# Kernel tuning notes

Measured on AMD Instinct MI355X. Metric: run time of the kernel, lower is better.

Reference implementation:

```python
import jax, jax.numpy as jnp
from jax import lax
import numpy as np

B, L, IN_DIM, HID, BINS = 1, 384, 41, 64, 63
ATTN_DIM, NUM_ANCHORS = 32, 32
NUM_CONV, ATTN_EVERY = 6, 2
SIGMA, EPS = 12.0, 1e-5
DILATIONS = [1, 2, 4, 8, 16]


def select_anchors(length, k):
    # deterministic 'stride' mode of select_anchors
    k = max(1, min(k, length))
    stride = max(1, length // k)
    idx = np.arange(0, length, stride)[:k]
    if idx.size < k:
        idx = np.concatenate([idx, np.full(k - idx.size, length - 1)])
    return jnp.asarray(idx, dtype=jnp.int32)


def conv2d(x, w, b, dilation=1):
    # x: (b, Cin, H, W), w: (Cout, Cin, kh, kw) -- 'same' padding like torch padding=dilation*(k//2)
    pad = dilation * (w.shape[-1] // 2)
    y = lax.conv_general_dilated(x, w, (1, 1), [(pad, pad), (pad, pad)],
                                 rhs_dilation=(dilation, dilation),
                                 dimension_numbers=('NCHW', 'OIHW', 'NCHW'))
    return y + b[None, :, None, None]


def instance_norm(x):
    # torch InstanceNorm2d(affine=False), eps=1e-5, per (b, c) over spatial dims
    mu = x.mean(axis=(2, 3), keepdims=True)
    var = x.var(axis=(2, 3), keepdims=True)
    return (x - mu) * lax.rsqrt(var + EPS)


def anchor_attention(pair, td, tq, anchors, wq, wl, wr, wvl, wvr, wo, wg, bg,
                     tg_w1, tg_b1, tg_w2, tg_b2):
    # pair: (b, L, L, d); td: (b, L, L); tq: (b,)
    q = pair @ wq                                    # (b, L, L, a)
    p_left = pair[:, :, anchors, :]                  # (b, L, K, d)
    p_right = pair[:, anchors, :, :]                 # (b, K, L, d)
    left = p_left @ wl                               # (b, L, K, a)
    right = p_right @ wr                             # (b, K, L, a)
    scores = jnp.einsum('bija,bika->bijk', q, left)
    scores = scores + jnp.einsum('bija,bkja->bijk', q, right)
    scores = scores / jnp.sqrt(jnp.float32(ATTN_DIM))
    # template bias, 'consistency' mode
    t_left = td[:, :, anchors]                       # (b, L, K)
    t_right = jnp.swapaxes(td[:, anchors, :], 1, 2)  # (b, L, K)
    t_sum = t_left[:, :, None, :] + t_right[:, None, :, :]  # (b, L, L, K)
    bias = -jnp.abs(t_sum - td[..., None]) / SIGMA
    # TemplateGate
    coverage = (td > 0).astype(jnp.float32).mean(axis=(1, 2))        # (b,)
    length_norm = jnp.full_like(coverage, td.shape[-1] / 512.0)
    feats = jnp.stack([coverage, tq, length_norm], axis=-1)          # (b, 3)
    g = jax.nn.sigmoid(jax.nn.relu(feats @ tg_w1 + tg_b1) @ tg_w2 + tg_b2)  # (b, 1)
    scores = scores + g[:, :, None, None] * bias
    attn = jax.nn.softmax(scores, axis=-1)
    v_left = p_left @ wvl                            # (b, L, K, a)
    v_right = p_right @ wvr                          # (b, K, L, a)
    update = jnp.einsum('bijk,bika->bija', attn, v_left)
    update = update + jnp.einsum('bijk,bkja->bija', attn, v_right)
    update = update @ wo                             # (b, L, L, d)
    gate = jax.nn.sigmoid(pair @ wg + bg)
    return pair + gate * update


def setup_inputs() -> dict:
    key = jax.random.key(0)
    ks = iter(jax.random.split(key, 40))

    def rn(shape, scale=0.05):
        return jax.random.normal(next(ks), shape, dtype=jnp.float32) * scale

    return dict(
        features=jax.random.normal(next(ks), (B, L, L, IN_DIM), dtype=jnp.float32),
        template_dist=jax.random.uniform(next(ks), (B, L, L), dtype=jnp.float32) * 20.0,
        template_quality=jax.random.uniform(next(ks), (B,), dtype=jnp.float32),
        in_w=rn((HID, IN_DIM, 1, 1)), in_b=rn((HID,)),
        conv1_w=rn((NUM_CONV, HID, HID, 3, 3)), conv1_b=rn((NUM_CONV, HID)),
        conv2_w=rn((NUM_CONV, HID, HID, 3, 3)), conv2_b=rn((NUM_CONV, HID)),
        wq=rn((HID, ATTN_DIM)), wl=rn((HID, ATTN_DIM)), wr=rn((HID, ATTN_DIM)),
        wvl=rn((HID, ATTN_DIM)), wvr=rn((HID, ATTN_DIM)), wo=rn((ATTN_DIM, HID)),
        wg=rn((HID, HID)), bg=rn((HID,)),
        tg_w1=rn((3, 16)), tg_b1=rn((16,)), tg_w2=rn((16, 1)), tg_b2=rn((1,)),
        dist_w=rn((BINS, HID, 3, 3)), dist_b=rn((BINS,)),
        cf_w1=rn((32, BINS, 3, 3)), cf_b1=rn((32,)),
        cf_w2=rn((32, 32, 3, 3)), cf_b2=rn((32,)),
        cf_w3=rn((1, 32, 1, 1)), cf_b3=rn((1,)),
    )


def reference(features, template_dist, template_quality, in_w, in_b,
              conv1_w, conv1_b, conv2_w, conv2_b,
              wq, wl, wr, wvl, wvr, wo, wg, bg, tg_w1, tg_b1, tg_w2, tg_b2,
              dist_w, dist_b, cf_w1, cf_b1, cf_w2, cf_b2, cf_w3, cf_b3):
    anchors = select_anchors(L, NUM_ANCHORS)
    x = conv2d(jnp.transpose(features, (0, 3, 1, 2)), in_w, in_b)  # (b, hid, L, L)
    num_attn = max(1, NUM_CONV // max(1, ATTN_EVERY))
    attn_added = 0
    for i in range(NUM_CONV):
        d = DILATIONS[i % len(DILATIONS)]
        res = x
        out = jax.nn.elu(instance_norm(conv2d(x, conv1_w[i], conv1_b[i], d)))
        out = instance_norm(conv2d(out, conv2_w[i], conv2_b[i], 1))
        x = jax.nn.elu(out + res)
        if (i + 1) % ATTN_EVERY == 0 and attn_added < num_attn:
            pair = jnp.transpose(x, (0, 2, 3, 1))
            pair = anchor_attention(pair, template_dist, template_quality, anchors,
                                    wq, wl, wr, wvl, wvr, wo, wg, bg,
                                    tg_w1, tg_b1, tg_w2, tg_b2)
            x = jnp.transpose(pair, (0, 3, 1, 2))
            attn_added += 1
    logits = conv2d(x, dist_w, dist_b)                       # (b, bins, L, L)
    logits = 0.5 * (logits + jnp.swapaxes(logits, 2, 3))     # symmetrize_pairs
    c = jax.nn.relu(conv2d(logits, cf_w1, cf_b1))
    c = jax.nn.relu(conv2d(c, cf_w2, cf_b2))
    confidence = jax.nn.sigmoid(conv2d(c, cf_w3, cf_b3))[:, 0]   # (b, L, L)
    distance_logits = jnp.transpose(logits, (0, 2, 3, 1))        # (b, L, L, bins)
    return distance_logits, confidence
```

## Files before the change

kernel.cpp:

```cpp
#include <hip/hip_runtime.h>
#include <math.h>

#define LDIM 384
#define NPIX (LDIM*LDIM)
#define NBINS 63

typedef __attribute__((ext_vector_type(8))) __bf16 bf16x8;
typedef __attribute__((ext_vector_type(4))) float floatx4;

__device__ __forceinline__ float sigf(float x){ return 1.f/(1.f+expf(-x)); }

__global__ __launch_bounds__(256) void prep_kernel(
    const float* __restrict__ c1w, const float* __restrict__ c2w,
    const float* __restrict__ dw, const float* __restrict__ cf1w,
    const float* __restrict__ cf2w, const float* __restrict__ wg,
    const float* __restrict__ wo, const float* __restrict__ wq,
    __bf16* __restrict__ Wf){
  int idx = blockIdx.x*256 + threadIdx.x;
  if (idx >= 515072) return;
  if (idx >= 506880){
    int rel, NT, NDIM; const float* src;
    if (idx < 510976){ rel = idx - 506880; src = wg; NT=4; NDIM=64; }
    else if (idx < 513024){ rel = idx - 510976; src = wo; NT=4; NDIM=64; }
    else { rel = idx - 513024; src = wq; NT=2; NDIM=32; }
    int j = rel & 7, lane = (rel>>3) & 63;
    int r2 = rel >> 9;
    int nt = r2 % NT, kc = r2 / NT;
    int k = kc*32 + (lane>>4)*8 + j;
    int n = nt*16 + (lane&15);
    Wf[idx] = (__bf16)src[(size_t)k*NDIM + n];
    return;
  }
  const float* src; int ICreal, OCreal, ICP, NT, rel;
  if (idx < 442368){
    int layer = idx / 36864; rel = idx - layer*36864;
    int i = layer >> 1;
    src = (layer & 1) ? (c2w + (size_t)i*36864) : (c1w + (size_t)i*36864);
    ICreal=64; OCreal=64; ICP=64; NT=4;
  } else if (idx < 479232){
    rel = idx - 442368; src = dw;   ICreal=64; OCreal=63; ICP=64; NT=4;
  } else if (idx < 497664){
    rel = idx - 479232; src = cf1w; ICreal=63; OCreal=32; ICP=64; NT=2;
  } else {
    rel = idx - 497664; src = cf2w; ICreal=32; OCreal=32; ICP=32; NT=2;
  }
  int j = rel & 7, lane = (rel>>3) & 63;
  int r2 = rel >> 9;
  int nt = r2 % NT; int r3 = r2 / NT;
  int KC = ICP/32;
  int kc = r3 % KC; int tap = r3 / KC;
  int k = kc*32 + (lane>>4)*8 + j;
  int n = nt*16 + (lane&15);
  float v = 0.f;
  if (k < ICreal && n < OCreal) v = src[((size_t)n*ICreal + k)*9 + tap];
  Wf[idx] = (__bf16)v;
}

template<int ICP, int NT, int D, int WAVES, bool NORM>
__global__ __launch_bounds__(WAVES*64) void mfma_conv(
    const __bf16* __restrict__ Ain, const __bf16* __restrict__ Wf,
    const float* __restrict__ bias, int OC_real,
    float* __restrict__ outF, __bf16* __restrict__ outP,
    int relu, const float* __restrict__ nstats, float* __restrict__ ostats){
  constexpr int KC = ICP/32;
  constexpr int W = WAVES*16;
  constexpr int T = WAVES*64;
  constexpr int SW = W + 2*D;
  constexpr int REC_B = ICP*4;
  constexpr int P_B = REC_B + 8;
  constexpr int PPX = ICP/8;
  constexpr int TOT1 = SW*PPX;
  constexpr int NC1 = (TOT1 + T - 1)/T;
  constexpr int OCS = NT*16;
  const int t = threadIdx.x;
  const int wave = t>>6, lane = t&63;
  const int q = lane>>4, col16 = lane&15;
  const int y = blockIdx.y;
  const int x0 = blockIdx.x*W;
  extern __shared__ __align__(16) char smem[];
  char* stage = smem;
  float* muS = (float*)(smem + (size_t)SW*P_B);

  if (NORM){
    if (t < 64){
      float s=0.f, sq=0.f;
      #pragma unroll
      for (int rp=0;rp<8;rp++){ s += nstats[rp*128 + t]; sq += nstats[rp*128 + 64 + t]; }
      float m = s*(1.f/NPIX);
      muS[t] = m;
      muS[64+t] = rsqrtf(sq*(1.f/NPIX) - m*m + 1e-5f);
    }
    __syncthreads();
  }

  floatx4 acc[NT];
  #pragma unroll
  for (int b=0;b<NT;b++){ floatx4 z = {0.f,0.f,0.f,0.f}; acc[b]=z; }

  #pragma unroll
  for (int ky=0; ky<3; ky++){
    const int yr = y + (ky-1)*D;
    uint4 vh[NC1], vl[NC1];
    #pragma unroll
    for (int k=0;k<NC1;k++){
      uint4 z = {0u,0u,0u,0u}; vh[k]=z; vl[k]=z;
      int pp = t + k*T;
      if (pp < TOT1){
        int px = pp/PPX; int sub = pp - px*PPX;
        int gx = x0 - D + px;
        if ((unsigned)yr < LDIM && (unsigned)gx < LDIM){
          const char* p = (const char*)Ain + ((size_t)yr*LDIM + gx)*REC_B + sub*16;
          vh[k] = *(const uint4*)p;
          vl[k] = *(const uint4*)(p + ICP*2);
        }
      }
    }
    if (NORM){
      #pragma unroll
      for (int k=0;k<NC1;k++){
        int pp = t + k*T;
        if (pp < TOT1){
          int px = pp/PPX; int sub = pp - px*PPX;
          int gx = x0 - D + px;
          if ((unsigned)yr < LDIM && (unsigned)gx < LDIM){
            int c0 = sub*8;
            floatx4 mua = *(floatx4*)(muS + c0), mub = *(floatx4*)(muS + c0 + 4);
            floatx4 rsa = *(floatx4*)(muS + 64 + c0), rsb = *(floatx4*)(muS + 64 + c0 + 4);
            __bf16* hp = (__bf16*)&vh[k]; __bf16* lp = (__bf16*)&vl[k];
            #pragma unroll
            for (int j=0;j<8;j++){
              float mu = (j<4) ? mua[j] : mub[j-4];
              float rs = (j<4) ? rsa[j] : rsb[j-4];
              float v = ((float)hp[j] + (float)lp[j] - mu)*rs;
              v = v>0.f ? v : expm1f(v);
              __bf16 h = (__bf16)v; hp[j]=h; lp[j]=(__bf16)(v-(float)h);
            }
          }
        }
      }
    }
    if (ky > 0) __syncthreads();
    #pragma unroll
    for (int k=0;k<NC1;k++){
      int pp = t + k*T;
      if (pp < TOT1){
        int px = pp/PPX; int sub = pp - px*PPX;
        char* sp = stage + (size_t)px*P_B + sub*16;
        *(uint4*)sp = vh[k];
        *(uint4*)(sp + ICP*2) = vl[k];
      }
    }
    __syncthreads();
    #pragma unroll
    for (int kx=0; kx<3; kx++){
      #pragma unroll
      for (int kc=0; kc<KC; kc++){
        int cl = wave*16 + col16 + kx*D;
        const char* ap = stage + (size_t)cl*P_B + (kc*4+q)*16;
        bf16x8 ah = *(const bf16x8*)ap;
        bf16x8 al = *(const bf16x8*)(ap + ICP*2);
        const __bf16* wkc = Wf + (size_t)((ky*3+kx)*KC + kc)*NT*512 + lane*8;
        #pragma unroll
        for (int nt=0; nt<NT; nt++){
          bf16x8 bfrag = *(const bf16x8*)(wkc + (size_t)nt*512);
          acc[nt] = __builtin_amdgcn_mfma_f32_16x16x32_bf16(ah, bfrag, acc[nt], 0,0,0);
          acc[nt] = __builtin_amdgcn_mfma_f32_16x16x32_bf16(al, bfrag, acc[nt], 0,0,0);
        }
      }
    }
  }

  float* red = (float*)stage;
  if (ostats) __syncthreads();
  #pragma unroll
  for (int nt=0; nt<NT; nt++){
    int oc = nt*16 + col16;
    float bv = (oc < OC_real) ? bias[oc] : 0.f;
    int pxb = x0 + wave*16 + q*4;
    float s=0.f, sq=0.f;
    #pragma unroll
    for (int r=0; r<4; r++){
      float vv = acc[nt][r] + bv;
      if (relu) vv = fmaxf(vv, 0.f);
      size_t pix = (size_t)y*LDIM + pxb + r;
      if (outF) outF[pix*OCS + oc] = vv;
      if (outP){
        __bf16 h = (__bf16)vv;
        __bf16* rec = outP + pix*(size_t)(OCS*2);
        rec[oc] = h; rec[OCS+oc] = (__bf16)(vv - (float)h);
      }
      s += vv; sq += vv*vv;
    }
    if (ostats){
      s  += __shfl_xor(s, 16);  s  += __shfl_xor(s, 32);
      sq += __shfl_xor(sq, 16); sq += __shfl_xor(sq, 32);
      if (q == 0){
        red[oc*WAVES + wave] = s;
        red[OCS*WAVES + oc*WAVES + wave] = sq;
      }
    }
  }
  if (ostats){
    __syncthreads();
    float* oslot = ostats + ((blockIdx.y & 7) << 7);
    if (t < OCS){
      float s=0.f, sq=0.f;
      #pragma unroll
      for (int w=0; w<WAVES; w++){
        s  += red[t*WAVES + w];
        sq += red[OCS*WAVES + t*WAVES + w];
      }
      atomicAdd(&oslot[t], s);
      atomicAdd(&oslot[64+t], sq);
    }
  }
}

__global__ __launch_bounds__(256) void in_proj_kernel(
    const float* __restrict__ feat, const float* __restrict__ w,
    const float* __restrict__ b, __bf16* __restrict__ PX){
  __shared__ float sf[16][41];
  __shared__ float sw[64*41];
  int t = threadIdx.x;
  size_t p0 = (size_t)blockIdx.x*16;
  float wv[11];
  #pragma unroll
  for (int k=0;k<11;k++){ int idx=t+k*256; wv[k] = (idx<2624) ? w[idx] : 0.f; }
  float fv[3];
  #pragma unroll
  for (int k=0;k<3;k++){ int idx=t+k*256; fv[k] = (idx<656) ? feat[p0*41 + idx] : 0.f; }
  #pragma unroll
  for (int k=0;k<11;k++){ int idx=t+k*256; if (idx<2624) sw[idx]=wv[k]; }
  #pragma unroll
  for (int k=0;k<3;k++){
    int idx=t+k*256;
    if (idx<656){ int p = idx/41, k2 = idx - p*41; sf[p][k2]=fv[k]; }
  }
  __syncthreads();
  #pragma unroll
  for (int k=0;k<4;k++){
    int item = t + k*256;
    int c = item&63, p = item>>6;
    float acc = b[c];
    #pragma unroll
    for (int kk=0;kk<41;kk++) acc += sf[p][kk]*sw[c*41+kk];
    __bf16 h = (__bf16)acc;
    __bf16* rec = PX + (p0+p)*128;
    rec[c] = h; rec[64+c] = (__bf16)(acc - (float)h);
  }
}

__global__ __launch_bounds__(256) void norm_res_elu_planes(
    const __bf16* __restrict__ U, __bf16* __restrict__ PX,
    const float* __restrict__ stats){
  size_t idx = (size_t)blockIdx.x*256 + threadIdx.x;
  size_t px = idx>>3; int c0 = (int)(idx&7)*8;
  const __bf16* ur = U + px*128;
  __bf16* xr = PX + px*128;
  uint4 uh = *(const uint4*)(ur + c0);
  uint4 ul = *(const uint4*)(ur + 64 + c0);
  uint4 xh = *(uint4*)(xr + c0);
  uint4 xl = *(uint4*)(xr + 64 + c0);
  __bf16* uhp=(__bf16*)&uh; __bf16* ulp=(__bf16*)&ul;
  __bf16* xhp=(__bf16*)&xh; __bf16* xlp=(__bf16*)&xl;
  float mu[8], rs[8];
  #pragma unroll
  for (int k=0;k<8;k++){
    int c = c0+k;
    float s=0.f, sq=0.f;
    #pragma unroll
    for (int rp=0;rp<8;rp++){ s += stats[rp*128 + c]; sq += stats[rp*128 + 64 + c]; }
    float m = s*(1.f/NPIX);
    mu[k]=m; rs[k]=rsqrtf(sq*(1.f/NPIX) - m*m + 1e-5f);
  }
  #pragma unroll
  for (int k=0;k<8;k++){
    float v = ((float)uhp[k] + (float)ulp[k] - mu[k])*rs[k]
            + ((float)xhp[k] + (float)xlp[k]);
    v = v>0.f ? v : expm1f(v);
    __bf16 h = (__bf16)v; xhp[k]=h; xlp[k]=(__bf16)(v-(float)h);
  }
  *(uint4*)(xr + c0) = xh;
  *(uint4*)(xr + 64 + c0) = xl;
}

__global__ __launch_bounds__(256) void g_partial_kernel(
    const float* __restrict__ td, float* __restrict__ GC){
  size_t base = (size_t)blockIdx.x*256;
  float cnt = (td[base + threadIdx.x] > 0.f) ? 1.f : 0.f;
  __shared__ float red[256];
  red[threadIdx.x]=cnt; __syncthreads();
  for (int st=128; st; st>>=1){
    if (threadIdx.x<st) red[threadIdx.x]+=red[threadIdx.x+st];
    __syncthreads();
  }
  if (threadIdx.x==0) atomicAdd(GC, red[0]);
}

__global__ void g_final_kernel(
    const float* __restrict__ GC, const float* __restrict__ tq,
    const float* __restrict__ w1, const float* __restrict__ b1,
    const float* __restrict__ w2, const float* __restrict__ b2,
    float* __restrict__ G){
  if (threadIdx.x==0){
    float f0 = GC[0]*(1.f/NPIX), f1 = tq[0], f2 = (float)LDIM/512.f;
    float z = b2[0];
    for (int j=0;j<16;j++){
      float h = f0*w1[j] + f1*w1[16+j] + f2*w1[32+j] + b1[j];
      z += (h>0.f?h:0.f)*w2[j];
    }
    G[0] = sigf(z);
  }
}

__global__ __launch_bounds__(256) void qproj_mfma_kernel(
    const __bf16* __restrict__ PX, const __bf16* __restrict__ WqF,
    __bf16* __restrict__ Qb){
  const int t=threadIdx.x, wave=t>>6, lane=t&63, q=lane>>4, col16=lane&15;
  const size_t p0=(size_t)blockIdx.x*128;
  __shared__ __bf16 Xhi[128*72];
  __shared__ __bf16 Xlo[128*72];
  uint4 sv[8];
  #pragma unroll
  for (int k=0;k<8;k++){
    int c=t+k*256;
    sv[k] = *(const uint4*)((const char*)PX + (p0 + (c>>4))*256 + (c&15)*16);
  }
  #pragma unroll
  for (int k=0;k<8;k++){
    int c=t+k*256; int px=c>>4, sub=c&15;
    *(uint4*)(((sub<8)?Xhi:Xlo) + px*72 + (sub&7)*8) = sv[k];
  }
  __syncthreads();
  floatx4 acc[2][2];
  #pragma unroll
  for (int a=0;a<2;a++)
    #pragma unroll
    for (int b=0;b<2;b++){ floatx4 z={0.f,0.f,0.f,0.f}; acc[a][b]=z; }
  #pragma unroll
  for (int kc=0;kc<2;kc++){
    bf16x8 ah[2], al[2];
    #pragma unroll
    for (int mt=0;mt<2;mt++){
      int row = wave*32 + mt*16 + col16;
      ah[mt] = *(const bf16x8*)(Xhi + row*72 + kc*32 + q*8);
      al[mt] = *(const bf16x8*)(Xlo + row*72 + kc*32 + q*8);
    }
    #pragma unroll
    for (int nt=0;nt<2;nt++){
      bf16x8 b = *(const bf16x8*)(WqF + (kc*2+nt)*512 + lane*8);
      acc[0][nt] = __builtin_amdgcn_mfma_f32_16x16x32_bf16(ah[0], b, acc[0][nt], 0,0,0);
      acc[1][nt] = __builtin_amdgcn_mfma_f32_16x16x32_bf16(ah[1], b, acc[1][nt], 0,0,0);
      acc[0][nt] = __builtin_amdgcn_mfma_f32_16x16x32_bf16(al[0], b, acc[0][nt], 0,0,0);
      acc[1][nt] = __builtin_amdgcn_mfma_f32_16x16x32_bf16(al[1], b, acc[1][nt], 0,0,0);
    }
  }
  #pragma unroll
  for (int mt=0;mt<2;mt++){
    size_t pxb = p0 + wave*32 + mt*16 + q*4;
    #pragma unroll
    for (int nt=0;nt<2;nt++){
      int oc = nt*16 + col16;
      #pragma unroll
      for (int r=0;r<4;r++)
        Qb[(pxb+r)*32 + oc] = (__bf16)acc[mt][nt][r];
    }
  }
}

__global__ __launch_bounds__(256) void proj_left_kernel(
    const __bf16* __restrict__ PX, const float* __restrict__ wl, const float* __restrict__ wvl,
    __bf16* __restrict__ leftb, __bf16* __restrict__ vleftTb){
  int i = blockIdx.x;
  __shared__ float xa[32][65];
  __shared__ float w1s[2048], w2s[2048];
  int c = threadIdx.x & 63;
  for (int a = threadIdx.x>>6; a<32; a+=4){
    const __bf16* rec = PX + ((size_t)i*LDIM + 12*a)*128;
    xa[a][c] = (float)rec[c] + (float)rec[64+c];
  }
  for (int idx=threadIdx.x; idx<2048; idx+=256){ w1s[idx]=wl[idx]; w2s[idx]=wvl[idx]; }
  __syncthreads();
  #pragma unroll
  for (int k=0;k<4;k++){
    int idx = threadIdx.x + k*256;
    int a = idx>>5, n = idx&31;
    float a1=0.f, a2=0.f;
    #pragma unroll
    for (int cc=0;cc<64;cc++){ float v=xa[a][cc]; a1+=v*w1s[cc*32+n]; a2+=v*w2s[cc*32+n]; }
    leftb  [(size_t)i*1024 + a*32 + n] = (__bf16)a1;
    vleftTb[(size_t)i*1024 + n*32 + a] = (__bf16)a2;
  }
}

__global__ __launch_bounds__(256) void proj_right_kernel(
    const __bf16* __restrict__ PX, const float* __restrict__ wr, const float* __restrict__ wvr,
    __bf16* __restrict__ rightb, __bf16* __restrict__ vrightTb){
  int a = blockIdx.y; int row = 12*a;
  int j0 = blockIdx.x*32;
  __shared__ float xr[32][65];
  __shared__ float w1s[2048], w2s[2048];
  for (int idx=threadIdx.x; idx<2048; idx+=256){ w1s[idx]=wr[idx]; w2s[idx]=wvr[idx]; }
// ... 258 lines not shown
    #pragma unroll
    for (int kk=0;kk<4;kk++) pu[kk]=(__bf16)uv[k][kk];
  }
  __syncthreads();
  floatx4 accg[2][4], accu[2][4];
  #pragma unroll
  for (int a=0;a<2;a++)
    #pragma unroll
    for (int b=0;b<4;b++){ floatx4 z={0.f,0.f,0.f,0.f}; accg[a][b]=z; accu[a][b]=z; }
  #pragma unroll
  for (int kc=0;kc<2;kc++){
    bf16x8 ah[2], al[2];
    #pragma unroll
    for (int mt=0;mt<2;mt++){
      int row = wave*32 + mt*16 + col16;
      ah[mt] = *(const bf16x8*)(Xhi + row*72 + kc*32 + q*8);
      al[mt] = *(const bf16x8*)(Xlo + row*72 + kc*32 + q*8);
    }
    #pragma unroll
    for (int nt=0;nt<4;nt++){
      bf16x8 b = *(const bf16x8*)(WgF + (kc*4+nt)*512 + lane*8);
      accg[0][nt] = __builtin_amdgcn_mfma_f32_16x16x32_bf16(ah[0], b, accg[0][nt], 0,0,0);
      accg[1][nt] = __builtin_amdgcn_mfma_f32_16x16x32_bf16(ah[1], b, accg[1][nt], 0,0,0);
      accg[0][nt] = __builtin_amdgcn_mfma_f32_16x16x32_bf16(al[0], b, accg[0][nt], 0,0,0);
      accg[1][nt] = __builtin_amdgcn_mfma_f32_16x16x32_bf16(al[1], b, accg[1][nt], 0,0,0);
    }
  }
  {
    bf16x8 au[2];
    #pragma unroll
    for (int mt=0;mt<2;mt++){
      int row = wave*32 + mt*16 + col16;
      au[mt] = *(const bf16x8*)(Ub + row*40 + q*8);
    }
    #pragma unroll
    for (int nt=0;nt<4;nt++){
      bf16x8 b = *(const bf16x8*)(WoF + nt*512 + lane*8);
      accu[0][nt] = __builtin_amdgcn_mfma_f32_16x16x32_bf16(au[0], b, accu[0][nt], 0,0,0);
      accu[1][nt] = __builtin_amdgcn_mfma_f32_16x16x32_bf16(au[1], b, accu[1][nt], 0,0,0);
    }
  }
  #pragma unroll
  for (int mt=0;mt<2;mt++){
    size_t pxb = p0 + wave*32 + mt*16 + q*4;
    #pragma unroll
    for (int nt=0;nt<4;nt++){
      int oc = nt*16 + col16;
      float bgv = bg[oc];
      #pragma unroll
      for (int r=0;r<4;r++){
        __bf16* rec = PX + (pxb+r)*128;
        float xv = (float)rec[oc] + (float)rec[64+oc];
        float g = sigf(accg[mt][nt][r] + bgv);
        float xn = xv + g*accu[mt][nt][r];
        __bf16 h = (__bf16)xn;
        rec[oc] = h; rec[64+oc] = (__bf16)(xn - (float)h);
      }
    }
  }
}

__global__ __launch_bounds__(256) void sym_kernel(
    const float* __restrict__ lg, __bf16* __restrict__ PS, float* __restrict__ dout){
  int i = blockIdx.y;
  int j = blockIdx.x*4 + (threadIdx.x>>6);
  int o = threadIdx.x & 63;
  float v = 0.5f*(lg[((size_t)i*LDIM+j)*64+o] + lg[((size_t)j*LDIM+i)*64+o]);
  size_t pix = (size_t)i*LDIM+j;
  __bf16 h = (__bf16)v;
  __bf16* rec = PS + pix*128;
  rec[o] = h; rec[64+o] = (__bf16)(v - (float)h);
  if (o<63) dout[pix*63+o] = v;
}

__global__ __launch_bounds__(256) void conf_kernel(
    const float* __restrict__ c2, const float* __restrict__ w,
    const float* __restrict__ b, float* __restrict__ out){
  int t = threadIdx.x;
  size_t pix = (size_t)blockIdx.x*8 + (t>>5);
  int c = t&31;
  float v = c2[pix*32 + c]*w[c];
  #pragma unroll
  for (int off=16; off; off>>=1) v += __shfl_xor(v, off);
  if (c==0) out[pix] = sigf(v + b[0]);
}

extern "C" void kernel_launch(void* const* d_in, const int* in_sizes, int n_in,
                              void* d_out, int out_size, void* d_ws, size_t ws_size,
                              hipStream_t stream){
  const float* feat = (const float*)d_in[0];
  const float* td   = (const float*)d_in[1];
  const float* tq   = (const float*)d_in[2];
  const float* in_w = (const float*)d_in[3];
  const float* in_b = (const float*)d_in[4];
  const float* c1w  = (const float*)d_in[5];
  const float* c1b  = (const float*)d_in[6];
  const float* c2w  = (const float*)d_in[7];
  const float* c2b  = (const float*)d_in[8];
  const float* wq   = (const float*)d_in[9];
  const float* wl   = (const float*)d_in[10];
  const float* wr   = (const float*)d_in[11];
  const float* wvl  = (const float*)d_in[12];
  const float* wvr  = (const float*)d_in[13];
  const float* wo   = (const float*)d_in[14];
  const float* wg   = (const float*)d_in[15];
  const float* bg   = (const float*)d_in[16];
  const float* tgw1 = (const float*)d_in[17];
  const float* tgb1 = (const float*)d_in[18];
  const float* tgw2 = (const float*)d_in[19];
  const float* tgb2 = (const float*)d_in[20];
  const float* dw   = (const float*)d_in[21];
  const float* db   = (const float*)d_in[22];
  const float* cf1w = (const float*)d_in[23];
  const float* cf1b = (const float*)d_in[24];
  const float* cf2w = (const float*)d_in[25];
  const float* cf2b = (const float*)d_in[26];
  const float* cf3w = (const float*)d_in[27];
  const float* cf3b = (const float*)d_in[28];

  float* ws = (float*)d_ws;
  const size_t BUF = (size_t)64*NPIX;
  float* R1 = ws;
  float* R2 = ws + BUF;
  float* R3 = ws + 2*BUF;
  float* STATS = ws + 3*BUF;
  float* G     = STATS + 12288;
  float* GC    = G + 1;
  __bf16* WF   = (__bf16*)(G + 16);
  __bf16* WGF  = WF + 506880;
  __bf16* WOF  = WF + 510976;
  __bf16* WQF  = WF + 513024;

  __bf16* PX = (__bf16*)R1;
  __bf16* PT = (__bf16*)R2;
  __bf16* PU = (__bf16*)R3;
  char* R2c = (char*)R2;
  __bf16* Qb       = (__bf16*)R2c;
  __bf16* ATTNB    = (__bf16*)(R2c +  9437184);
  __bf16* ATTNTB   = (__bf16*)(R2c + 18874368);
  __bf16* LEFTB    = (__bf16*)(R2c + 28311552);
  __bf16* RIGHTB   = (__bf16*)(R2c + 29097984);
  __bf16* VLEFTTB  = (__bf16*)(R2c + 29884416);
  __bf16* VRIGHTTB = (__bf16*)(R2c + 30670848);
  float* S   = R3;
  float* UPD = R3 + (size_t)32*NPIX;

  hipMemsetAsync(STATS, 0, (12288 + 16)*sizeof(float), stream);
  prep_kernel<<<2012, 256, 0, stream>>>(c1w, c2w, dw, cf1w, cf2w, wg, wo, wq, WF);
  g_partial_kernel<<<576, 256, 0, stream>>>(td, GC);
  g_final_kernel<<<1, 64, 0, stream>>>(GC, tq, tgw1, tgb1, tgw2, tgb2, G);

  in_proj_kernel<<<9216, 256, 0, stream>>>(feat, in_w, in_b, PX);

#define CONV_LDS(DD) ((64+2*(DD))*264)

#define CONV2_NORM(i) \
  mfma_conv<64,4,1,4,true><<<dim3(6,LDIM), 256, CONV_LDS(1)+512, stream>>>( \
      PT, WF + (size_t)(2*(i)+1)*36864, c2b + (i)*64, 64, \
      nullptr, PU, 0, STATS + (2*(i))*1024, STATS + (2*(i)+1)*1024); \
  norm_res_elu_planes<<<4608, 256, 0, stream>>>(PU, PX, STATS + (2*(i)+1)*1024);

#define CONV1(i, DD) \
  mfma_conv<64,4,DD,4,false><<<dim3(6,LDIM), 256, CONV_LDS(DD), stream>>>( \
      PX, WF + (size_t)(2*(i))*36864, c1b + (i)*64, 64, \
      nullptr, PT, 0, nullptr, STATS + (2*(i))*1024);

#define ATTN_BLOCK \
  qproj_mfma_kernel<<<1152, 256, 0, stream>>>(PX, WQF, Qb); \
  proj_left_kernel<<<384, 256, 0, stream>>>(PX, wl, wvl, LEFTB, VLEFTTB); \
  proj_right_kernel<<<dim3(12,32), 256, 0, stream>>>(PX, wr, wvr, RIGHTB, VRIGHTTB); \
  attn_s1_kernel<<<dim3(3,LDIM), 256, 0, stream>>>(Qb, LEFTB, S); \
  attn_s2_kernel<<<dim3(3,LDIM), 256, 0, stream>>>(Qb, RIGHTB, S); \
  attn_soft_kernel<<<dim3(3,LDIM), 128, 0, stream>>>(S, td, G, ATTNB, ATTNTB); \
  attn_u1_kernel<<<dim3(3,LDIM), 256, 0, stream>>>(ATTNB, VLEFTTB, UPD); \
  attn_u2_kernel<<<dim3(3,LDIM), 256, 0, stream>>>(ATTNTB, VRIGHTTB, UPD); \
  gate_mfma_kernel<<<1152, 256, 0, stream>>>(PX, UPD, WGF, WOF, bg);

  CONV1(0, 1)   CONV2_NORM(0)
  CONV1(1, 2)   CONV2_NORM(1)  ATTN_BLOCK
  CONV1(2, 4)   CONV2_NORM(2)
  CONV1(3, 8)   CONV2_NORM(3)  ATTN_BLOCK
  CONV1(4, 16)  CONV2_NORM(4)
  CONV1(5, 1)   CONV2_NORM(5)  ATTN_BLOCK

  mfma_conv<64,4,1,4,false><<<dim3(6,LDIM), 256, CONV_LDS(1), stream>>>(
      PX, WF + 442368, db, 63, R3, nullptr, 0, nullptr, nullptr);
  sym_kernel<<<dim3(96,LDIM), 256, 0, stream>>>(R3, PT, (float*)d_out);
  mfma_conv<64,2,1,4,false><<<dim3(6,LDIM), 256, CONV_LDS(1), stream>>>(
      PT, WF + 479232, cf1b, 32, nullptr, PX, 1, nullptr, nullptr);
  mfma_conv<32,2,1,4,false><<<dim3(6,LDIM), 256, (64+2)*136, stream>>>(
      PX, WF + 497664, cf2b, 32, R3, nullptr, 1, nullptr, nullptr);
  conf_kernel<<<18432, 256, 0, stream>>>(R3, cf3w, cf3b, (float*)d_out + (size_t)NPIX*NBINS);
}
```

Measured before the change: 1.559 ms.

## Compute four output rows per conv block with rolling input-row reuse and prefetch

The MFMA conv kernel now has each block compute R=4 output rows spaced by the dilation, so each staged input row feeds up to three output rows' accumulators instead of being reloaded three times. The next input row is prefetched into registers while the current one is consumed (double-buffered registers). The grid shrinks from 384 to 96 row-blocks. This cuts global loads and LDS staging but raises register pressure (4x accumulators plus double buffers) and reduces the block count, which may hurt occupancy.

```diff
diff --git a/kernel.cpp b/kernel.cpp
--- a/kernel.cpp
+++ b/kernel.cpp
@@ -56,7 +56,7 @@
   Wf[idx] = (__bf16)v;
 }
 
-template<int ICP, int NT, int D, int WAVES, bool NORM>
+template<int ICP, int NT, int D, int WAVES, int R, bool NORM>
 __global__ __launch_bounds__(WAVES*64) void mfma_conv(
     const __bf16* __restrict__ Ain, const __bf16* __restrict__ Wf,
     const float* __restrict__ bias, int OC_real,
@@ -75,7 +75,9 @@
   const int t = threadIdx.x;
   const int wave = t>>6, lane = t&63;
   const int q = lane>>4, col16 = lane&15;
-  const int y = blockIdx.y;
+  const int by = blockIdx.y;
+  const int res = by % D, chain = by / D;
+  const int y0 = res + chain*(R*D);
   const int x0 = blockIdx.x*W;
   extern __shared__ __align__(16) char smem[];
   char* stage = smem;
@@ -93,61 +95,83 @@
     __syncthreads();
   }
 
-  floatx4 acc[NT];
-  #pragma unroll
-  for (int b=0;b<NT;b++){ floatx4 z = {0.f,0.f,0.f,0.f}; acc[b]=z; }
-
-  #pragma unroll
-  for (int ky=0; ky<3; ky++){
-    const int yr = y + (ky-1)*D;
-    uint4 vh[NC1], vl[NC1];
+  floatx4 acc[R][NT];
+  #pragma unroll
+  for (int i=0;i<R;i++)
+    #pragma unroll
+    for (int b=0;b<NT;b++){ floatx4 z = {0.f,0.f,0.f,0.f}; acc[i][b]=z; }
+
+  int pxk[NC1], gxk[NC1]; bool actk[NC1];
+  #pragma unroll
+  for (int k=0;k<NC1;k++){
+    int pp = t + k*T;
+    actk[k] = (pp < TOT1);
+    int px = pp / PPX;
+    pxk[k] = px;
+    gxk[k] = x0 - D + px;
+  }
+
+  uint4 vh[2][NC1], vl[2][NC1];
+
+  {
+    const int yr = y0 - D;
     #pragma unroll
     for (int k=0;k<NC1;k++){
-      uint4 z = {0u,0u,0u,0u}; vh[k]=z; vl[k]=z;
-      int pp = t + k*T;
-      if (pp < TOT1){
-        int px = pp/PPX; int sub = pp - px*PPX;
-        int gx = x0 - D + px;
-        if ((unsigned)yr < LDIM && (unsigned)gx < LDIM){
-          const char* p = (const char*)Ain + ((size_t)yr*LDIM + gx)*REC_B + sub*16;
-          vh[k] = *(const uint4*)p;
-          vl[k] = *(const uint4*)(p + ICP*2);
-        }
-      }
-    }
+      uint4 z = {0u,0u,0u,0u}; vh[0][k]=z; vl[0][k]=z;
+      if (actk[k] && (unsigned)yr < LDIM && (unsigned)gxk[k] < LDIM){
+        int sub = (t + k*T) & (PPX-1);
+        const char* p = (const char*)Ain + ((size_t)yr*LDIM + gxk[k])*REC_B + sub*16;
+        vh[0][k] = *(const uint4*)p;
+        vl[0][k] = *(const uint4*)(p + ICP*2);
+      }
+    }
+  }
+
+  #pragma unroll
+  for (int p=0; p<R+2; ++p){
+    const int cs = p & 1;
+    const int yr = y0 + (p-1)*D;
     if (NORM){
       #pragma unroll
       for (int k=0;k<NC1;k++){
-        int pp = t + k*T;
-        if (pp < TOT1){
-          int px = pp/PPX; int sub = pp - px*PPX;
-          int gx = x0 - D + px;
-          if ((unsigned)yr < LDIM && (unsigned)gx < LDIM){
-            int c0 = sub*8;
-            floatx4 mua = *(floatx4*)(muS + c0), mub = *(floatx4*)(muS + c0 + 4);
-            floatx4 rsa = *(floatx4*)(muS + 64 + c0), rsb = *(floatx4*)(muS + 64 + c0 + 4);
-            __bf16* hp = (__bf16*)&vh[k]; __bf16* lp = (__bf16*)&vl[k];
-            #pragma unroll
-            for (int j=0;j<8;j++){
-              float mu = (j<4) ? mua[j] : mub[j-4];
-              float rs = (j<4) ? rsa[j] : rsb[j-4];
-              float v = ((float)hp[j] + (float)lp[j] - mu)*rs;
-              v = v>0.f ? v : expm1f(v);
-              __bf16 h = (__bf16)v; hp[j]=h; lp[j]=(__bf16)(v-(float)h);
-            }
+        if (actk[k] && (unsigned)yr < LDIM && (unsigned)gxk[k] < LDIM){
+          int c0 = ((t + k*T) & (PPX-1))*8;
+          floatx4 mua = *(floatx4*)(muS + c0), mub = *(floatx4*)(muS + c0 + 4);
+          floatx4 rsa = *(floatx4*)(muS + 64 + c0), rsb = *(floatx4*)(muS + 64 + c0 + 4);
+          __bf16* hp = (__bf16*)&vh[cs][k]; __bf16* lp = (__bf16*)&vl[cs][k];
+          #pragma unroll
+          for (int j=0;j<8;j++){
+            float mu = (j<4) ? mua[j] : mub[j-4];
+            float rs = (j<4) ? rsa[j] : rsb[j-4];
+            float v = ((float)hp[j] + (float)lp[j] - mu)*rs;
+            v = v>0.f ? v : expm1f(v);
+            __bf16 h = (__bf16)v; hp[j]=h; lp[j]=(__bf16)(v-(float)h);
           }
         }
       }
     }
-    if (ky > 0) __syncthreads();
+    if (p > 0) __syncthreads();
     #pragma unroll
     for (int k=0;k<NC1;k++){
-      int pp = t + k*T;
-      if (pp < TOT1){
-        int px = pp/PPX; int sub = pp - px*PPX;
-        char* sp = stage + (size_t)px*P_B + sub*16;
-        *(uint4*)sp = vh[k];
-        *(uint4*)(sp + ICP*2) = vl[k];
+      if (actk[k]){
+        int sub = (t + k*T) & (PPX-1);
+        char* sp = stage + (size_t)pxk[k]*P_B + sub*16;
+        *(uint4*)sp = vh[cs][k];
+        *(uint4*)(sp + ICP*2) = vl[cs][k];
+      }
+    }
+    if (p < R+1){
+      const int yn = y0 + p*D;
+      const int ns = cs ^ 1;
+      #pragma unroll
+      for (int k=0;k<NC1;k++){
+        uint4 z = {0u,0u,0u,0u}; vh[ns][k]=z; vl[ns][k]=z;
+        if (actk[k] && (unsigned)yn < LDIM && (unsigned)gxk[k] < LDIM){
+          int sub = (t + k*T) & (PPX-1);
+          const char* pp2 = (const char*)Ain + ((size_t)yn*LDIM + gxk[k])*REC_B + sub*16;
+          vh[ns][k] = *(const uint4*)pp2;
+          vl[ns][k] = *(const uint4*)(pp2 + ICP*2);
+        }
       }
     }
     __syncthreads();
@@ -159,39 +183,55 @@
         const char* ap = stage + (size_t)cl*P_B + (kc*4+q)*16;
         bf16x8 ah = *(const bf16x8*)ap;
         bf16x8 al = *(const bf16x8*)(ap + ICP*2);
-        const __bf16* wkc = Wf + (size_t)((ky*3+kx)*KC + kc)*NT*512 + lane*8;
         #pragma unroll
-        for (int nt=0; nt<NT; nt++){
-          bf16x8 bfrag = *(const bf16x8*)(wkc + (size_t)nt*512);
-          acc[nt] = __builtin_amdgcn_mfma_f32_16x16x32_bf16(ah, bfrag, acc[nt], 0,0,0);
-          acc[nt] = __builtin_amdgcn_mfma_f32_16x16x32_bf16(al, bfrag, acc[nt], 0,0,0);
+        for (int i=0; i<R; i++){
+          if (i > p || p - i > 2) continue;
+          const int ky = p - i;
+          const __bf16* wkc = Wf + (size_t)((ky*3+kx)*KC + kc)*NT*512 + lane*8;
+          #pragma unroll
+          for (int nt=0; nt<NT; nt++){
+            bf16x8 bfrag = *(const bf16x8*)(wkc + (size_t)nt*512);
+            acc[i][nt] = __builtin_amdgcn_mfma_f32_16x16x32_bf16(ah, bfrag, acc[i][nt], 0,0,0);
+            acc[i][nt] = __builtin_amdgcn_mfma_f32_16x16x32_bf16(al, bfrag, acc[i][nt], 0,0,0);
+          }
         }
       }
     }
   }
 
   float* red = (float*)stage;
+  float sAcc[NT], sqAcc[NT];
+  #pragma unroll
+  for (int nt=0;nt<NT;nt++){ sAcc[nt]=0.f; sqAcc[nt]=0.f; }
   if (ostats) __syncthreads();
   #pragma unroll
-  for (int nt=0; nt<NT; nt++){
-    int oc = nt*16 + col16;
-    float bv = (oc < OC_real) ? bias[oc] : 0.f;
-    int pxb = x0 + wave*16 + q*4;
-    float s=0.f, sq=0.f;
-    #pragma unroll
-    for (int r=0; r<4; r++){
-      float vv = acc[nt][r] + bv;
-      if (relu) vv = fmaxf(vv, 0.f);
-      size_t pix = (size_t)y*LDIM + pxb + r;
-      if (outF) outF[pix*OCS + oc] = vv;
-      if (outP){
-        __bf16 h = (__bf16)vv;
-        __bf16* rec = outP + pix*(size_t)(OCS*2);
-        rec[oc] = h; rec[OCS+oc] = (__bf16)(vv - (float)h);
-      }
-      s += vv; sq += vv*vv;
-    }
-    if (ostats){
+  for (int i=0;i<R;i++){
+    const int y = y0 + i*D;
+    #pragma unroll
+    for (int nt=0; nt<NT; nt++){
+      int oc = nt*16 + col16;
+      float bv = (oc < OC_real) ? bias[oc] : 0.f;
+      int pxb = x0 + wave*16 + q*4;
+      #pragma unroll
+      for (int r=0; r<4; r++){
+        float vv = acc[i][nt][r] + bv;
+        if (relu) vv = fmaxf(vv, 0.f);
+        size_t pix = (size_t)y*LDIM + pxb + r;
+        if (outF) outF[pix*OCS + oc] = vv;
+        if (outP){
+          __bf16 h = (__bf16)vv;
+          __bf16* rec = outP + pix*(size_t)(OCS*2);
+          rec[oc] = h; rec[OCS+oc] = (__bf16)(vv - (float)h);
+        }
+        sAcc[nt] += vv; sqAcc[nt] += vv*vv;
+      }
+    }
+  }
+  if (ostats){
+    #pragma unroll
+    for (int nt=0; nt<NT; nt++){
+      int oc = nt*16 + col16;
+      float s = sAcc[nt], sq = sqAcc[nt];
       s  += __shfl_xor(s, 16);  s  += __shfl_xor(s, 32);
       sq += __shfl_xor(sq, 16); sq += __shfl_xor(sq, 32);
       if (q == 0){
@@ -199,8 +239,6 @@
         red[OCS*WAVES + oc*WAVES + wave] = sq;
       }
     }
-  }
-  if (ostats){
     __syncthreads();
     float* oslot = ostats + ((blockIdx.y & 7) << 7);
     if (t < OCS){
@@ -815,13 +853,13 @@
 #define CONV_LDS(DD) ((64+2*(DD))*264)
 
 #define CONV2_NORM(i) \
-  mfma_conv<64,4,1,4,true><<<dim3(6,LDIM), 256, CONV_LDS(1)+512, stream>>>( \
+  mfma_conv<64,4,1,4,4,true><<<dim3(6,96), 256, CONV_LDS(1)+512, stream>>>( \
       PT, WF + (size_t)(2*(i)+1)*36864, c2b + (i)*64, 64, \
       nullptr, PU, 0, STATS + (2*(i))*1024, STATS + (2*(i)+1)*1024); \
   norm_res_elu_planes<<<4608, 256, 0, stream>>>(PU, PX, STATS + (2*(i)+1)*1024);
 
 #define CONV1(i, DD) \
-  mfma_conv<64,4,DD,4,false><<<dim3(6,LDIM), 256, CONV_LDS(DD), stream>>>( \
+  mfma_conv<64,4,DD,4,4,false><<<dim3(6,96), 256, CONV_LDS(DD), stream>>>( \
       PX, WF + (size_t)(2*(i))*36864, c1b + (i)*64, 64, \
       nullptr, PT, 0, nullptr, STATS + (2*(i))*1024);
 
@@ -843,12 +881,12 @@
   CONV1(4, 16)  CONV2_NORM(4)
   CONV1(5, 1)   CONV2_NORM(5)  ATTN_BLOCK
 
-  mfma_conv<64,4,1,4,false><<<dim3(6,LDIM), 256, CONV_LDS(1), stream>>>(
+  mfma_conv<64,4,1,4,4,false><<<dim3(6,96), 256, CONV_LDS(1), stream>>>(
       PX, WF + 442368, db, 63, R3, nullptr, 0, nullptr, nullptr);
   sym_kernel<<<dim3(96,LDIM), 256, 0, stream>>>(R3, PT, (float*)d_out);
-  mfma_conv<64,2,1,4,false><<<dim3(6,LDIM), 256, CONV_LDS(1), stream>>>(
+  mfma_conv<64,2,1,4,4,false><<<dim3(6,96), 256, CONV_LDS(1), stream>>>(
       PT, WF + 479232, cf1b, 32, nullptr, PX, 1, nullptr, nullptr);
-  mfma_conv<32,2,1,4,false><<<dim3(6,LDIM), 256, (64+2)*136, stream>>>(
+  mfma_conv<32,2,1,4,4,false><<<dim3(6,96), 256, (64+2)*136, stream>>>(
       PX, WF + 497664, cf2b, 32, R3, nullptr, 1, nullptr, nullptr);
   conf_kernel<<<18432, 256, 0, stream>>>(R3, cf3w, cf3b, (float*)d_out + (size_t)NPIX*NBINS);
 }
```

New measurement: 2.303 ms. 47.7% more time.

## Drop LDS staging in conv; read input fragments directly from global memory

Applied to the files above, without the earlier changes.

The MFMA conv kernel no longer stages an input row strip into shared memory with barriers. Each lane now loads its A fragments straight from global memory, per tap and per channel chunk, and relies on cache for reuse across the three horizontal taps. The fused instance-norm plus ELU applied to the conv2 input is split out into a separate in-place elementwise kernel that runs before conv2. This removes LDS traffic and syncs and frees shared memory for occupancy, but it adds redundant global/L2 loads and an extra full-tensor read/write pass per layer.

```diff
diff --git a/kernel.cpp b/kernel.cpp
--- a/kernel.cpp
+++ b/kernel.cpp
@@ -56,42 +56,22 @@
   Wf[idx] = (__bf16)v;
 }
 
-template<int ICP, int NT, int D, int WAVES, bool NORM>
+template<int ICP, int NT, int D, int WAVES>
 __global__ __launch_bounds__(WAVES*64) void mfma_conv(
     const __bf16* __restrict__ Ain, const __bf16* __restrict__ Wf,
     const float* __restrict__ bias, int OC_real,
     float* __restrict__ outF, __bf16* __restrict__ outP,
-    int relu, const float* __restrict__ nstats, float* __restrict__ ostats){
+    int relu, float* __restrict__ ostats){
   constexpr int KC = ICP/32;
-  constexpr int W = WAVES*16;
-  constexpr int T = WAVES*64;
-  constexpr int SW = W + 2*D;
+  constexpr int OCS = NT*16;
   constexpr int REC_B = ICP*4;
-  constexpr int P_B = REC_B + 8;
-  constexpr int PPX = ICP/8;
-  constexpr int TOT1 = SW*PPX;
-  constexpr int NC1 = (TOT1 + T - 1)/T;
-  constexpr int OCS = NT*16;
+  __shared__ float red[OCS*WAVES*2];
   const int t = threadIdx.x;
   const int wave = t>>6, lane = t&63;
   const int q = lane>>4, col16 = lane&15;
   const int y = blockIdx.y;
-  const int x0 = blockIdx.x*W;
-  extern __shared__ __align__(16) char smem[];
-  char* stage = smem;
-  float* muS = (float*)(smem + (size_t)SW*P_B);
-
-  if (NORM){
-    if (t < 64){
-      float s=0.f, sq=0.f;
-      #pragma unroll
-      for (int rp=0;rp<8;rp++){ s += nstats[rp*128 + t]; sq += nstats[rp*128 + 64 + t]; }
-      float m = s*(1.f/NPIX);
-      muS[t] = m;
-      muS[64+t] = rsqrtf(sq*(1.f/NPIX) - m*m + 1e-5f);
-    }
-    __syncthreads();
-  }
+  const int x0 = blockIdx.x*(WAVES*16);
+  const int gx0 = x0 + wave*16 + col16;
 
   floatx4 acc[NT];
   #pragma unroll
@@ -100,78 +80,39 @@
   #pragma unroll
   for (int ky=0; ky<3; ky++){
     const int yr = y + (ky-1)*D;
-    uint4 vh[NC1], vl[NC1];
-    #pragma unroll
-    for (int k=0;k<NC1;k++){
-      uint4 z = {0u,0u,0u,0u}; vh[k]=z; vl[k]=z;
-      int pp = t + k*T;
-      if (pp < TOT1){
-        int px = pp/PPX; int sub = pp - px*PPX;
-        int gx = x0 - D + px;
-        if ((unsigned)yr < LDIM && (unsigned)gx < LDIM){
-          const char* p = (const char*)Ain + ((size_t)yr*LDIM + gx)*REC_B + sub*16;
-          vh[k] = *(const uint4*)p;
-          vl[k] = *(const uint4*)(p + ICP*2);
+    if ((unsigned)yr < LDIM){
+      const char* rowb = (const char*)Ain + (size_t)yr*LDIM*REC_B + q*16;
+      #pragma unroll
+      for (int kx=0; kx<3; kx++){
+        const int gx = gx0 + (kx-1)*D;
+        bf16x8 ah[KC], al[KC];
+        #pragma unroll
+        for (int kc=0;kc<KC;kc++){
+          #pragma unroll
+          for (int j=0;j<8;j++){ ah[kc][j]=(__bf16)0.f; al[kc][j]=(__bf16)0.f; }
         }
-      }
-    }
-    if (NORM){
-      #pragma unroll
-      for (int k=0;k<NC1;k++){
-        int pp = t + k*T;
-        if (pp < TOT1){
-          int px = pp/PPX; int sub = pp - px*PPX;
-          int gx = x0 - D + px;
-          if ((unsigned)yr < LDIM && (unsigned)gx < LDIM){
-            int c0 = sub*8;
-            floatx4 mua = *(floatx4*)(muS + c0), mub = *(floatx4*)(muS + c0 + 4);
-            floatx4 rsa = *(floatx4*)(muS + 64 + c0), rsb = *(floatx4*)(muS + 64 + c0 + 4);
-            __bf16* hp = (__bf16*)&vh[k]; __bf16* lp = (__bf16*)&vl[k];
-            #pragma unroll
-            for (int j=0;j<8;j++){
-              float mu = (j<4) ? mua[j] : mub[j-4];
-              float rs = (j<4) ? rsa[j] : rsb[j-4];
-              float v = ((float)hp[j] + (float)lp[j] - mu)*rs;
-              v = v>0.f ? v : expm1f(v);
-              __bf16 h = (__bf16)v; hp[j]=h; lp[j]=(__bf16)(v-(float)h);
-            }
+        if ((unsigned)gx < LDIM){
+          const char* p = rowb + (size_t)gx*REC_B;
+          #pragma unroll
+          for (int kc=0;kc<KC;kc++){
+            ah[kc] = *(const bf16x8*)(p + kc*64);
+            al[kc] = *(const bf16x8*)(p + kc*64 + ICP*2);
+          }
+        }
+        #pragma unroll
+        for (int kc=0;kc<KC;kc++){
+          const __bf16* wkc = Wf + (size_t)((ky*3+kx)*KC + kc)*NT*512 + lane*8;
+          #pragma unroll
+          for (int nt=0; nt<NT; nt++){
+            bf16x8 bfrag = *(const bf16x8*)(wkc + (size_t)nt*512);
+            acc[nt] = __builtin_amdgcn_mfma_f32_16x16x32_bf16(ah[kc], bfrag, acc[nt], 0,0,0);
+            acc[nt] = __builtin_amdgcn_mfma_f32_16x16x32_bf16(al[kc], bfrag, acc[nt], 0,0,0);
           }
         }
       }
     }
-    if (ky > 0) __syncthreads();
-    #pragma unroll
-    for (int k=0;k<NC1;k++){
-      int pp = t + k*T;
-      if (pp < TOT1){
-        int px = pp/PPX; int sub = pp - px*PPX;
-        char* sp = stage + (size_t)px*P_B + sub*16;
-        *(uint4*)sp = vh[k];
-        *(uint4*)(sp + ICP*2) = vl[k];
-      }
-    }
-    __syncthreads();
-    #pragma unroll
-    for (int kx=0; kx<3; kx++){
-      #pragma unroll
-      for (int kc=0; kc<KC; kc++){
-        int cl = wave*16 + col16 + kx*D;
-        const char* ap = stage + (size_t)cl*P_B + (kc*4+q)*16;
-        bf16x8 ah = *(const bf16x8*)ap;
-        bf16x8 al = *(const bf16x8*)(ap + ICP*2);
-        const __bf16* wkc = Wf + (size_t)((ky*3+kx)*KC + kc)*NT*512 + lane*8;
-        #pragma unroll
-        for (int nt=0; nt<NT; nt++){
-          bf16x8 bfrag = *(const bf16x8*)(wkc + (size_t)nt*512);
-          acc[nt] = __builtin_amdgcn_mfma_f32_16x16x32_bf16(ah, bfrag, acc[nt], 0,0,0);
-          acc[nt] = __builtin_amdgcn_mfma_f32_16x16x32_bf16(al, bfrag, acc[nt], 0,0,0);
-        }
-      }
-    }
-  }
-
-  float* red = (float*)stage;
-  if (ostats) __syncthreads();
+  }
+
   #pragma unroll
   for (int nt=0; nt<NT; nt++){
     int oc = nt*16 + col16;
@@ -248,6 +189,34 @@
     __bf16* rec = PX + (p0+p)*128;
     rec[c] = h; rec[64+c] = (__bf16)(acc - (float)h);
   }
+}
+
+__global__ __launch_bounds__(256) void norm_elu_planes(
+    __bf16* __restrict__ U, const float* __restrict__ stats){
+  size_t idx = (size_t)blockIdx.x*256 + threadIdx.x;
+  size_t px = idx>>3; int c0 = (int)(idx&7)*8;
+  __bf16* ur = U + px*128;
+  uint4 uh = *(const uint4*)(ur + c0);
+  uint4 ul = *(const uint4*)(ur + 64 + c0);
+  __bf16* uhp=(__bf16*)&uh; __bf16* ulp=(__bf16*)&ul;
+  float mu[8], rs[8];
+  #pragma unroll
+  for (int k=0;k<8;k++){
+    int c = c0+k;
+    float s=0.f, sq=0.f;
+    #pragma unroll
+    for (int rp=0;rp<8;rp++){ s += stats[rp*128 + c]; sq += stats[rp*128 + 64 + c]; }
+    float m = s*(1.f/NPIX);
+    mu[k]=m; rs[k]=rsqrtf(sq*(1.f/NPIX) - m*m + 1e-5f);
+  }
+  #pragma unroll
+  for (int k=0;k<8;k++){
+    float v = ((float)uhp[k] + (float)ulp[k] - mu[k])*rs[k];
+    v = v>0.f ? v : expm1f(v);
+    __bf16 h = (__bf16)v; uhp[k]=h; ulp[k]=(__bf16)(v-(float)h);
+  }
+  *(uint4*)(ur + c0) = uh;
+  *(uint4*)(ur + 64 + c0) = ul;
 }
 
 __global__ __launch_bounds__(256) void norm_res_elu_planes(
@@ -812,18 +781,17 @@
 
   in_proj_kernel<<<9216, 256, 0, stream>>>(feat, in_w, in_b, PX);
 
-#define CONV_LDS(DD) ((64+2*(DD))*264)
-
 #define CONV2_NORM(i) \
-  mfma_conv<64,4,1,4,true><<<dim3(6,LDIM), 256, CONV_LDS(1)+512, stream>>>( \
+  norm_elu_planes<<<4608, 256, 0, stream>>>(PT, STATS + (2*(i))*1024); \
+  mfma_conv<64,4,1,4><<<dim3(6,LDIM), 256, 0, stream>>>( \
       PT, WF + (size_t)(2*(i)+1)*36864, c2b + (i)*64, 64, \
-      nullptr, PU, 0, STATS + (2*(i))*1024, STATS + (2*(i)+1)*1024); \
+      nullptr, PU, 0, STATS + (2*(i)+1)*1024); \
   norm_res_elu_planes<<<4608, 256, 0, stream>>>(PU, PX, STATS + (2*(i)+1)*1024);
 
 #define CONV1(i, DD) \
-  mfma_conv<64,4,DD,4,false><<<dim3(6,LDIM), 256, CONV_LDS(DD), stream>>>( \
+  mfma_conv<64,4,DD,4><<<dim3(6,LDIM), 256, 0, stream>>>( \
       PX, WF + (size_t)(2*(i))*36864, c1b + (i)*64, 64, \
-      nullptr, PT, 0, nullptr, STATS + (2*(i))*1024);
+      nullptr, PT, 0, STATS + (2*(i))*1024);
 
 #define ATTN_BLOCK \
   qproj_mfma_kernel<<<1152, 256, 0, stream>>>(PX, WQF, Qb); \
@@ -843,12 +811,12 @@
   CONV1(4, 16)  CONV2_NORM(4)
   CONV1(5, 1)   CONV2_NORM(5)  ATTN_BLOCK
 
-  mfma_conv<64,4,1,4,false><<<dim3(6,LDIM), 256, CONV_LDS(1), stream>>>(
-      PX, WF + 442368, db, 63, R3, nullptr, 0, nullptr, nullptr);
+  mfma_conv<64,4,1,4><<<dim3(6,LDIM), 256, 0, stream>>>(
+      PX, WF + 442368, db, 63, R3, nullptr, 0, nullptr);
   sym_kernel<<<dim3(96,LDIM), 256, 0, stream>>>(R3, PT, (float*)d_out);
-  mfma_conv<64,2,1,4,false><<<dim3(6,LDIM), 256, CONV_LDS(1), stream>>>(
-      PT, WF + 479232, cf1b, 32, nullptr, PX, 1, nullptr, nullptr);
-  mfma_conv<32,2,1,4,false><<<dim3(6,LDIM), 256, (64+2)*136, stream>>>(
-      PX, WF + 497664, cf2b, 32, R3, nullptr, 1, nullptr, nullptr);
+  mfma_conv<64,2,1,4><<<dim3(6,LDIM), 256, 0, stream>>>(
+      PT, WF + 479232, cf1b, 32, nullptr, PX, 1, nullptr);
+  mfma_conv<32,2,1,4><<<dim3(6,LDIM), 256, 0, stream>>>(
+      PX, WF + 497664, cf2b, 32, R3, nullptr, 1, nullptr);
   conf_kernel<<<18432, 256, 0, stream>>>(R3, cf3w, cf3b, (float*)d_out + (size_t)NPIX*NBINS);
 }
```

Result: slower. 1.750 ms (+12.2%).
